# Kernel tuning notes

Hardware: AMD Instinct MI355X
Metric: run time of the kernel (lower is better)

The kernel has to match this reference:

```python
import jax, jax.numpy as jnp
import numpy as np

# NF4 16-level codebook (bitsandbytes values)
NF4_CODEBOOK = jnp.array([
    -1.0, -0.6961928009986877, -0.5250730514526367, -0.39491748809814453,
    -0.28444138169288635, -0.18477343022823334, -0.09105003625154495, 0.0,
    0.07958029955625534, 0.16093020141124725, 0.24611230194568634,
    0.33791524171829224, 0.44070982933044434, 0.5626170039176941,
    0.7229568362236328, 1.0], dtype=jnp.float32)

GROUP = 64      # quant_group_size for NF4
R = 16          # LoRA rank
ALPHA = 16      # lora_alpha -> scaling = ALPHA / R = 1.0
E, H, I, T, TOPK = 8, 2048, 1024, 512, 2


def nf4_dequant_gkn(packed, scales, K, N):
    """packed: [E, K//2, N] uint8-valued ints (two 4-bit codes per byte along K).
    scales: [E, K//GROUP, N] float32 per-group absmax. Returns [E, K, N] fp32."""
    e = packed.shape[0]
    lo = packed & 15
    hi = (packed >> 4) & 15
    codes = jnp.stack([lo, hi], axis=2).reshape(e, K, N)      # interleave along K
    w = NF4_CODEBOOK[codes]                                    # [E, K, N]
    w = w.reshape(e, K // GROUP, GROUP, N) * scales[:, :, None, :]
    return w.reshape(e, K, N)


def setup_inputs() -> dict:
    key = jax.random.key(0)
    ks = jax.random.split(key, 16)
    lora_std = 1.0 / np.sqrt(H)
    return {
        "x": jax.random.normal(ks[0], (T, H), jnp.float32),
        "topk_idx": jax.random.randint(ks[1], (T, TOPK), 0, E, jnp.int32),
        "topk_w": jax.random.uniform(ks[2], (T, TOPK), jnp.float32),
        "gate_packed": jax.random.randint(ks[3], (E, H // 2, I), 0, 256, jnp.int32),
        "gate_scales": jax.random.uniform(ks[4], (E, H // GROUP, I), jnp.float32) * 0.02,
        "up_packed": jax.random.randint(ks[5], (E, H // 2, I), 0, 256, jnp.int32),
        "up_scales": jax.random.uniform(ks[6], (E, H // GROUP, I), jnp.float32) * 0.02,
        "down_packed": jax.random.randint(ks[7], (E, I // 2, H), 0, 256, jnp.int32),
        "down_scales": jax.random.uniform(ks[8], (E, I // GROUP, H), jnp.float32) * 0.02,
        "gate_A": jax.random.normal(ks[9], (E, H, R), jnp.float32) * lora_std,
        "gate_B": jax.random.normal(ks[10], (E, R, I), jnp.float32) * 0.02,
        "up_A": jax.random.normal(ks[11], (E, H, R), jnp.float32) * lora_std,
        "up_B": jax.random.normal(ks[12], (E, R, I), jnp.float32) * 0.02,
        "down_A": jax.random.normal(ks[13], (E, I, R), jnp.float32) * lora_std,
        "down_B": jax.random.normal(ks[14], (E, R, H), jnp.float32) * 0.02,
    }


def reference(x, topk_idx, topk_w, gate_packed, gate_scales, up_packed, up_scales,
              down_packed, down_scales, gate_A, gate_B, up_A, up_B, down_A, down_B):
    scaling = ALPHA / R
    # Dequantized NF4 base + LoRA delta, GKN layout [E, K, N]
    Wg = nf4_dequant_gkn(gate_packed, gate_scales, H, I) + scaling * jnp.einsum('ekr,ern->ekn', gate_A, gate_B)
    Wu = nf4_dequant_gkn(up_packed, up_scales, H, I) + scaling * jnp.einsum('ekr,ern->ekn', up_A, up_B)
    Wd = nf4_dequant_gkn(down_packed, down_scales, I, H) + scaling * jnp.einsum('ekr,ern->ekn', down_A, down_B)
    # Grouped GEMM (dense-over-experts reference): SwiGLU per expert
    g = jnp.einsum('th,ehi->eti', x, Wg)          # [E, T, I]
    u = jnp.einsum('th,ehi->eti', x, Wu)
    h = jax.nn.silu(g) * u
    o = jnp.einsum('eti,eih->eth', h, Wd)         # [E, T, H]
    # Routing combine: per-token per-expert weight from top-k assignments
    w_te = jnp.sum((topk_idx[:, :, None] == jnp.arange(E)) * topk_w[:, :, None], axis=1)  # [T, E]
    return jnp.einsum('eth,te->th', o, w_te)
```

## Files before the change

### kernel.cpp

```cpp
#include <hip/hip_runtime.h>
#include <math.h>

#define NE 8
#define NH 2048
#define NI 1024
#define NT 512
#define NTOPK 2
#define NR 16
#define NGROUP 64
#define NPAIR (NT*NTOPK)

#define SPG 1040
#define SPD 528

typedef short bf16x8 __attribute__((ext_vector_type(8)));
typedef float f32x16 __attribute__((ext_vector_type(16)));
typedef unsigned int u32;

#define MFMA32 __builtin_amdgcn_mfma_f32_32x32x16_bf16

__device__ const float NF4_TAB[16] = {
    -1.0f, -0.6961928009986877f, -0.5250730514526367f, -0.39491748809814453f,
    -0.28444138169288635f, -0.18477343022823334f, -0.09105003625154495f, 0.0f,
    0.07958029955625534f, 0.16093020141124725f, 0.24611230194568634f,
    0.33791524171829224f, 0.44070982933044434f, 0.5626170039176941f,
    0.7229568362236328f, 1.0f};

#define OFF_EXPOFF 0
#define OFF_TOK    256
#define OFF_EXP    4352
#define OFF_W      8448
#define OFF_XAG    12544
#define OFF_XAU    45312
#define OFF_HA     78080
#define OFF_XCT    131072
#define OFF_GU     4325376
#define OFF_HT     10616832
#define OFF_CG     12713984
#define OFF_CU     21233664
#define OFF_CD     29753344

__device__ inline u32 f2bf(float f) {
    return (__float_as_uint(f) + 0x8000u) >> 16;
}
__device__ inline u32 bfpack2(float a, float b) {
    return ((__float_as_uint(a) + 0x8000u) >> 16) |
           ((__float_as_uint(b) + 0x8000u) & 0xFFFF0000u);
}
__device__ inline bf16x8 asbf(uint4 w) {
    union { uint4 u; bf16x8 b; } c; c.u = w; return c.b;
}
__device__ inline bf16x8 bfzero() { return asbf(make_uint4(0,0,0,0)); }
__device__ inline float bf2f(u32 v) { return __uint_as_float(v << 16); }

__device__ __forceinline__ void stage16(const void* g, void* l) {
    __builtin_amdgcn_global_load_lds(
        (const __attribute__((address_space(1))) u32*)g,
        (__attribute__((address_space(3))) u32*)l, 16, 0, 0);
}
#define WAITV0()  asm volatile("s_waitcnt vmcnt(0)" ::: "memory")

__global__ __launch_bounds__(256) void k_cmp3(const u32* __restrict__ gin,
                                              const u32* __restrict__ uin,
                                              const u32* __restrict__ din,
                                              unsigned char* __restrict__ cg,
                                              unsigned char* __restrict__ cu,
                                              unsigned char* __restrict__ cd,
                                              const int* __restrict__ idx,
                                              const float* __restrict__ w,
                                              int* expert_off, int* ptok,
                                              int* pexp, float* pw) {
    __shared__ u32 tile32[32][33];
    __shared__ int cnt[NE], off2[NE + 1], cur[NE];
    int tid = threadIdx.x;
    int z = blockIdx.z;

    if (z == 24) {
        if (blockIdx.x || blockIdx.y) return;
        if (tid < NE) cnt[tid] = 0;
        __syncthreads();
        int e4[4]; float w4[4];
        #pragma unroll
        for (int i = 0; i < 4; ++i) {
            int pr = tid * 4 + i;
            e4[i] = idx[pr]; w4[i] = w[pr];
            atomicAdd(&cnt[e4[i]], 1);
        }
        __syncthreads();
        if (tid == 0) {
            off2[0] = 0;
            for (int i = 0; i < NE; i++) off2[i + 1] = off2[i] + cnt[i];
        }
        __syncthreads();
        if (tid < NE) cur[tid] = off2[tid];
        __syncthreads();
        #pragma unroll
        for (int i = 0; i < 4; ++i) {
            int pr = tid * 4 + i;
            int pos = atomicAdd(&cur[e4[i]], 1);
            ptok[pos] = pr >> 1; pexp[pos] = e4[i]; pw[pos] = w4[i];
        }
        if (tid <= NE) expert_off[tid] = off2[tid];
        return;
    }

    const u32* in; unsigned char* out; int K2, N, SP, e;
    if (z < 2 * NE) {
        e = z >> 1;
        in = (z & 1) ? uin : gin; out = (z & 1) ? cu : cg;
        K2 = NH / 2; N = NI; SP = SPG;
        if ((int)blockIdx.x >= N / 128) return;
    } else {
        e = z - 2 * NE;
        in = din; out = cd;
        K2 = NI / 2; N = NH; SP = SPD;
        if ((int)blockIdx.y >= K2 / 32) return;
    }
    int kp0 = blockIdx.y * 32, c0 = blockIdx.x * 128;

    int c16 = tid & 31, rr = tid >> 5;
    const u32* ip = in + (size_t)e * K2 * N + (size_t)kp0 * N + c0;
    #pragma unroll
    for (int pass = 0; pass < 4; ++pass) {
        int r = pass * 8 + rr;
        uint4 v = *(const uint4*)(ip + (size_t)r * N + c16 * 4);
        tile32[r][c16] = (v.x & 255) | ((v.y & 255) << 8) |
                         ((v.z & 255) << 16) | ((v.w & 255) << 24);
    }
    __syncthreads();

    int col = tid >> 1, half = tid & 1;
    int cq = col >> 2, sh = (col & 3) * 8;
    uint4 ow; u32* op = &ow.x;
    #pragma unroll
    for (int i = 0; i < 4; ++i) {
        int base = half * 16 + i * 4;
        u32 b0 = (tile32[base + 0][cq] >> sh) & 255;
        u32 b1 = (tile32[base + 1][cq] >> sh) & 255;
        u32 b2 = (tile32[base + 2][cq] >> sh) & 255;
        u32 b3 = (tile32[base + 3][cq] >> sh) & 255;
        op[i] = b0 | (b1 << 8) | (b2 << 16) | (b3 << 24);
    }
    *(uint4*)(out + (size_t)e * N * SP + (size_t)(c0 + col) * SP
              + kp0 + half * 16) = ow;
}

__global__ __launch_bounds__(256) void k_xA(const float* __restrict__ x,
                                            const float* __restrict__ gA,
                                            const float* __restrict__ uA,
                                            const int* __restrict__ ptok,
                                            const int* __restrict__ pexp,
                                            unsigned short* __restrict__ xcT,
                                            unsigned short* __restrict__ xAg,
                                            unsigned short* __restrict__ xAu) {
    __shared__ float xs[NH];
    __shared__ float red[2][64][17];
    int p = blockIdx.x;
    int t = ptok[p], e = pexp[p];
    int tid = threadIdx.x;

    int k = tid * 8;
    const float* xr = x + (size_t)t * NH + k;
    float4 v0 = *(const float4*)xr;
    float4 v1 = *(const float4*)(xr + 4);
    uint4 w;
    w.x = bfpack2(v0.x, v0.y); w.y = bfpack2(v0.z, v0.w);
    w.z = bfpack2(v1.x, v1.y); w.w = bfpack2(v1.z, v1.w);
    *(uint4*)(xcT + ((size_t)(k >> 3) * NPAIR + p) * 8) = w;
    *(float4*)(xs + k) = v0;
    *(float4*)(xs + k + 4) = v1;
    __syncthreads();

    int ch = tid & 63, rg = tid >> 6;
    const float* gAr = gA + (size_t)e * NH * NR + rg * 4;
    const float* uAr = uA + (size_t)e * NH * NR + rg * 4;
    float4 sg = make_float4(0.f, 0.f, 0.f, 0.f);
    float4 su = make_float4(0.f, 0.f, 0.f, 0.f);
    #pragma unroll 4
    for (int jj = 0; jj < NH / 64; ++jj) {
        int j = jj * 64 + ch;
        float xv = xs[j];
        float4 ga = *(const float4*)(gAr + (size_t)j * NR);
        float4 ua = *(const float4*)(uAr + (size_t)j * NR);
        sg.x += xv * ga.x; sg.y += xv * ga.y; sg.z += xv * ga.z; sg.w += xv * ga.w;
        su.x += xv * ua.x; su.y += xv * ua.y; su.z += xv * ua.z; su.w += xv * ua.w;
    }
    red[0][ch][rg * 4 + 0] = sg.x; red[0][ch][rg * 4 + 1] = sg.y;
    red[0][ch][rg * 4 + 2] = sg.z; red[0][ch][rg * 4 + 3] = sg.w;
    red[1][ch][rg * 4 + 0] = su.x; red[1][ch][rg * 4 + 1] = su.y;
    red[1][ch][rg * 4 + 2] = su.z; red[1][ch][rg * 4 + 3] = su.w;
    __syncthreads();
    for (int st = 32; st >= 1; st >>= 1) {
        if (ch < st) {
            #pragma unroll
            for (int i = 0; i < 4; ++i) {
                red[0][ch][rg * 4 + i] += red[0][ch + st][rg * 4 + i];
                red[1][ch][rg * 4 + i] += red[1][ch + st][rg * 4 + i];
            }
        }
        __syncthreads();
    }
    if (tid < 16)
        xAg[p * NR + tid] = (unsigned short)f2bf(red[0][0][tid]);
    else if (tid < 32)
        xAu[p * NR + (tid - 16)] = (unsigned short)f2bf(red[1][0][tid - 16]);
}

__global__ __launch_bounds__(64, 3) void k_gu(
    const unsigned short* __restrict__ xcT,
    const unsigned char* __restrict__ cgp, const float* __restrict__ gsc,
    const unsigned char* __restrict__ cup, const float* __restrict__ usc,
    const float* __restrict__ gB, const float* __restrict__ uB,
    const unsigned short* __restrict__ xAg, const unsigned short* __restrict__ xAu,
    const int* __restrict__ expert_off,
    unsigned short* __restrict__ gu)
{
    __shared__ u32 lut[256];
    __shared__ float sclb[32][32];

    int lane = threadIdx.x;
    int q = lane >> 5, cw = lane & 31;
    for (int i = lane; i < 256; i += 64)
        lut[i] = bfpack2(NF4_TAB[i & 15], NF4_TAB[(i >> 4) & 15]);

    int e = blockIdx.x;
    int c0 = blockIdx.y * 32;
    int mat = blockIdx.z & 1;
    int rt = blockIdx.z >> 1;
    const unsigned char* cp = mat ? cup : cgp;
    const float* scp = mat ? usc : gsc;
    const float* Bp = mat ? uB : gB;
    const unsigned short* xA = mat ? xAu : xAg;

    int off = expert_off[e];
    int cnt = expert_off[e + 1] - off;
    int colg = c0 + cw;

    {
        const float* sg = scp + (size_t)e * (NH / NGROUP) * NI + c0;
        #pragma unroll
        for (int g = 0; g < 4; ++g)
            stage16(sg + (size_t)(g * 8 + (lane >> 3)) * NI + ((lane & 7) << 2),
                    &sclb[g * 8][0]);
    }
    WAITV0();

    const unsigned char* cb = cp + ((size_t)e * NI + colg) * SPG + (q << 4);

    const int NS = NH / 64;
    for (int s0 = rt * 32; s0 < cnt; s0 += 128) {
        int rr = s0 + cw; if (rr > cnt - 1) rr = cnt - 1;
        int prow = off + rr;

        auto loadC = [&](uint4& c, int s) {
            c = *(const uint4*)(cb + (s << 5));
        };
        auto loadA = [&](bf16x8* d, int s) {
            #pragma unroll
            for (int ks = 0; ks < 4; ++ks)
                d[ks] = *(const bf16x8*)(xcT +
                            ((size_t)((s << 3) + (q << 2) + ks) * NPAIR + prow) * 8);
        };

        uint4 C0, C1;
        bf16x8 Aa[4], Ab[4];
        f32x16 acc;
        #pragma unroll
        for (int i = 0; i < 16; ++i) acc[i] = 0.f;

        auto compute = [&](const uint4& cv, const bf16x8* Ar, float scl) {
            const u32* cd = &cv.x;
            f32x16 t;
            #pragma unroll
            for (int i = 0; i < 16; ++i) t[i] = 0.f;
            #pragma unroll
            for (int ks = 0; ks < 4; ++ks) {
                u32 d = cd[ks];
                uint4 w4;
                w4.x = lut[d & 255];
                w4.y = lut[(d >> 8) & 255];
                w4.z = lut[(d >> 16) & 255];
                w4.w = lut[d >> 24];
                t = MFMA32(Ar[ks], asbf(w4), t, 0, 0, 0);
            }
            #pragma unroll
            for (int i = 0; i < 16; ++i) acc[i] += scl * t[i];
        };

        loadC(C0, 0); loadA(Aa, 0);
        loadC(C1, 1); loadA(Ab, 1);
        for (int s = 0; s < NS; s += 2) {
            compute(C0, Aa, sclb[s][cw]);
            if (s + 2 < NS) { loadC(C0, s + 2); loadA(Aa, s + 2); }
            compute(C1, Ab, sclb[s + 1][cw]);
            if (s + 3 < NS) { loadC(C1, s + 3); loadA(Ab, s + 3); }
        }

        {
            bf16x8 la = bfzero();
            if (s0 + cw < cnt)
                la = *(const bf16x8*)(xA + (size_t)(off + s0 + cw) * NR + (q << 3));
            const float* Bq = Bp + ((size_t)e * NR + (q << 3)) * NI + colg;
            uint4 w4; u32* wp = &w4.x;
            #pragma unroll
            for (int i = 0; i < 4; ++i)
                wp[i] = bfpack2(Bq[(2 * i) * NI], Bq[(2 * i + 1) * NI]);
            acc = MFMA32(la, asbf(w4), acc, 0, 0, 0);
        }
        unsigned short* outb = gu + (size_t)mat * NPAIR * NI;
        #pragma unroll
        for (int reg = 0; reg < 16; ++reg) {
            int rloc = (reg & 3) + 8 * (reg >> 2) + (q << 2);
            if (s0 + rloc < cnt)
                outb[(size_t)(off + s0 + rloc) * NI + colg] =
                    (unsigned short)f2bf(acc[reg]);
        }
    }
}

__global__ __launch_bounds__(256) void k_hsw(const unsigned short* __restrict__ gu,
                                             const float* __restrict__ dA,
                                             const int* __restrict__ pexp,
                                             unsigned short* __restrict__ hT,
                                             unsigned short* __restrict__ hA) {
    __shared__ float hs[NI];
    __shared__ float red[64][17];
    int p = blockIdx.x, e = pexp[p];
    int tid = threadIdx.x;

    int i = tid * 4;
    uint2 gv = *(const uint2*)(gu + (size_t)p * NI + i);
    uint2 uv = *(const uint2*)(gu + (size_t)NPAIR * NI + (size_t)p * NI + i);
    const u32* gp = &gv.x; const u32* up = &uv.x;
    uint2 hv; u32* hp = &hv.x;
    float4 h4;
    {
        float g0 = bf2f(gp[0] & 0xFFFFu), g1 = bf2f(gp[0] >> 16);
        float u0 = bf2f(up[0] & 0xFFFFu), u1 = bf2f(up[0] >> 16);
        h4.x = g0 * u0 / (1.f + __expf(-g0));
        h4.y = g1 * u1 / (1.f + __expf(-g1));
        hp[0] = bfpack2(h4.x, h4.y);
        float g2 = bf2f(gp[1] & 0xFFFFu), g3 = bf2f(gp[1] >> 16);
        float u2 = bf2f(up[1] & 0xFFFFu), u3 = bf2f(up[1] >> 16);
        h4.z = g2 * u2 / (1.f + __expf(-g2));
        h4.w = g3 * u3 / (1.f + __expf(-g3));
        hp[1] = bfpack2(h4.z, h4.w);
    }
    *(uint2*)(hT + ((size_t)(i >> 3) * NPAIR + p) * 8 + (i & 7)) = hv;
    *(float4*)(hs + i) = h4;
    __syncthreads();

    int ch = tid & 63, rg = tid >> 6;
    const float* dAr = dA + (size_t)e * NI * NR + rg * 4;
    float4 sv = make_float4(0.f, 0.f, 0.f, 0.f);
    #pragma unroll 4
    for (int jj = 0; jj < NI / 64; ++jj) {
        int j = jj * 64 + ch;
        float hvv = hs[j];
        float4 da = *(const float4*)(dAr + (size_t)j * NR);
        sv.x += hvv * da.x; sv.y += hvv * da.y;
        sv.z += hvv * da.z; sv.w += hvv * da.w;
    }
    red[ch][rg * 4 + 0] = sv.x; red[ch][rg * 4 + 1] = sv.y;
    red[ch][rg * 4 + 2] = sv.z; red[ch][rg * 4 + 3] = sv.w;
    __syncthreads();
    for (int st = 32; st >= 1; st >>= 1) {
        if (ch < st) {
            #pragma unroll
            for (int i2 = 0; i2 < 4; ++i2)
                red[ch][rg * 4 + i2] += red[ch + st][rg * 4 + i2];
        }
        __syncthreads();
    }
    if (tid < 16) hA[p * NR + tid] = (unsigned short)f2bf(red[0][tid]);
}

__global__ __launch_bounds__(64, 3) void k_dn(
    const unsigned short* __restrict__ hT,
    const unsigned char* __restrict__ cdp, const float* __restrict__ dsc,
    const float* __restrict__ dB,
    const unsigned short* __restrict__ hA,
    const int* __restrict__ expert_off, const int* __restrict__ ptok,
    const float* __restrict__ pw,
    float* __restrict__ out)
{
    __shared__ u32 lut[256];
    __shared__ float sclb[16][32];

    int lane = threadIdx.x;
    int q = lane >> 5, cw = lane & 31;
    for (int i = lane; i < 256; i += 64)
        lut[i] = bfpack2(NF4_TAB[i & 15], NF4_TAB[(i >> 4) & 15]);

    int e = blockIdx.x;
    int c0 = blockIdx.y * 32;
    int rt = blockIdx.z;

    int off = expert_off[e];
    int cnt = expert_off[e + 1] - off;
    int colg = c0 + cw;

    {
        const float* sg = dsc + (size_t)e * (NI / NGROUP) * NH + c0;
        #pragma unroll
        for (int g = 0; g < 2; ++g)
            stage16(sg + (size_t)(g * 8 + (lane >> 3)) * NH + ((lane & 7) << 2),
                    &sclb[g * 8][0]);
    }
    WAITV0();

    const unsigned char* cb = cdp + ((size_t)e * NH + colg) * SPD + (q << 4);

    const int NS = NI / 64;
    for (int s0 = rt * 32; s0 < cnt; s0 += 128) {
        int rr = s0 + cw; if (rr > cnt - 1) rr = cnt - 1;
        int prow = off + rr;

        auto loadC = [&](uint4& c, int s) {
            c = *(const uint4*)(cb + (s << 5));
        };
        auto loadA = [&](bf16x8* d, int s) {
            #pragma unroll
            for (int ks = 0; ks < 4; ++ks)
                d[ks] = *(const bf16x8*)(hT +
                            ((size_t)((s << 3) + (q << 2) + ks) * NPAIR + prow) * 8);
        };

        uint4 C0, C1;
        bf16x8 Aa[4], Ab[4];
        f32x16 acc;
        #pragma unroll
        for (int i = 0; i < 16; ++i) acc[i] = 0.f;

        auto compute = [&](const uint4& cv, const bf16x8* Ar, float scl) {
            const u32* cd = &cv.x;
            f32x16 t;
            #pragma unroll
            for (int i = 0; i < 16; ++i) t[i] = 0.f;
            #pragma unroll
            for (int ks = 0; ks < 4; ++ks) {
                u32 d = cd[ks];
                uint4 w4;
                w4.x = lut[d & 255];
                w4.y = lut[(d >> 8) & 255];
                w4.z = lut[(d >> 16) & 255];
                w4.w = lut[d >> 24];
                t = MFMA32(Ar[ks], asbf(w4), t, 0, 0, 0);
            }
            #pragma unroll
            for (int i = 0; i < 16; ++i) acc[i] += scl * t[i];
        };

        loadC(C0, 0); loadA(Aa, 0);
        loadC(C1, 1); loadA(Ab, 1);
        for (int s = 0; s < NS; s += 2) {
            compute(C0, Aa, sclb[s][cw]);
            if (s + 2 < NS) { loadC(C0, s + 2); loadA(Aa, s + 2); }
            compute(C1, Ab, sclb[s + 1][cw]);
            if (s + 3 < NS) { loadC(C1, s + 3); loadA(Ab, s + 3); }
        }

        {
            bf16x8 la = bfzero();
            if (s0 + cw < cnt)
                la = *(const bf16x8*)(hA + (size_t)(off + s0 + cw) * NR + (q << 3));
            const float* Bq = dB + ((size_t)e * NR + (q << 3)) * NH + colg;
            uint4 w4; u32* wp = &w4.x;
            #pragma unroll
            for (int i = 0; i < 4; ++i)
                wp[i] = bfpack2(Bq[(2 * i) * NH], Bq[(2 * i + 1) * NH]);
            acc = MFMA32(la, asbf(w4), acc, 0, 0, 0);
        }
        #pragma unroll
        for (int reg = 0; reg < 16; ++reg) {
            int rloc = (reg & 3) + 8 * (reg >> 2) + (q << 2);
            if (s0 + rloc < cnt) {
                int p = off + s0 + rloc;
                atomicAdd(&out[(size_t)ptok[p] * NH + colg], acc[reg] * pw[p]);
            }
        }
    }
}

extern "C" void kernel_launch(void* const* d_in, const int* in_sizes, int n_in,
                              void* d_out, int out_size, void* d_ws,
                              size_t ws_size, hipStream_t stream) {
    const float* x = (const float*)d_in[0];
    const int* topk_idx = (const int*)d_in[1];
    const float* topk_w = (const float*)d_in[2];
    const int* gate_packed = (const int*)d_in[3];
    const float* gate_scales = (const float*)d_in[4];
    const int* up_packed = (const int*)d_in[5];
    const float* up_scales = (const float*)d_in[6];
    const int* down_packed = (const int*)d_in[7];
    const float* down_scales = (const float*)d_in[8];
    const float* gate_A = (const float*)d_in[9];
    const float* gate_B = (const float*)d_in[10];
    const float* up_A = (const float*)d_in[11];
    const float* up_B = (const float*)d_in[12];
    const float* down_A = (const float*)d_in[13];
    const float* down_B = (const float*)d_in[14];
    float* out = (float*)d_out;

    char* ws = (char*)d_ws;
    int* expert_off = (int*)(ws + OFF_EXPOFF);
    int* ptok = (int*)(ws + OFF_TOK);
    int* pexp = (int*)(ws + OFF_EXP);
    float* pw = (float*)(ws + OFF_W);
    unsigned short* xAg = (unsigned short*)(ws + OFF_XAG);
    unsigned short* xAu = (unsigned short*)(ws + OFF_XAU);
    unsigned short* hA = (unsigned short*)(ws + OFF_HA);
    unsigned short* xcT = (unsigned short*)(ws + OFF_XCT);
    unsigned short* gu = (unsigned short*)(ws + OFF_GU);
    unsigned short* hT = (unsigned short*)(ws + OFF_HT);
    unsigned char* cg = (unsigned char*)(ws + OFF_CG);
    unsigned char* cu = (unsigned char*)(ws + OFF_CU);
    unsigned char* cd = (unsigned char*)(ws + OFF_CD);

    hipMemsetAsync(d_out, 0, (size_t)NT * NH * sizeof(float), stream);

    k_cmp3<<<dim3(16, 32, 25), 256, 0, stream>>>(
        (const u32*)gate_packed, (const u32*)up_packed, (const u32*)down_packed,
        cg, cu, cd, topk_idx, topk_w, expert_off, ptok, pexp, pw);

    k_xA<<<NPAIR, 256, 0, stream>>>(x, gate_A, up_A, ptok, pexp, xcT, xAg, xAu);
    k_gu<<<dim3(NE, NI / 32, 8), 64, 0, stream>>>(
        xcT, cg, gate_scales, cu, up_scales, gate_B, up_B,
        xAg, xAu, expert_off, gu);
    k_hsw<<<NPAIR, 256, 0, stream>>>(gu, down_A, pexp, hT, hA);
    k_dn<<<dim3(NE, NH / 32, 4), 64, 0, stream>>>(
        hT, cd, down_scales, down_B, hA, expert_off, ptok, pw, out);
}
```

Before: 271.1 us.

## Pre-dequantize NF4 weights to scaled bf16 in prepass, simplify GEMM inner loops

New measurement: 632.8 us. +133.4%, slower.

```diff
diff --git a/kernel.cpp b/kernel.cpp
--- a/kernel.cpp
+++ b/kernel.cpp
@@ -9,9 +9,6 @@
 #define NR 16
 #define NGROUP 64
 #define NPAIR (NT*NTOPK)
-
-#define SPG 1040
-#define SPD 528
 
 typedef short bf16x8 __attribute__((ext_vector_type(8)));
 typedef float f32x16 __attribute__((ext_vector_type(16)));
@@ -35,10 +32,10 @@
 #define OFF_HA     78080
 #define OFF_XCT    131072
 #define OFF_GU     4325376
-#define OFF_HT     10616832
-#define OFF_CG     12713984
-#define OFF_CU     21233664
-#define OFF_CD     29753344
+#define OFF_HT     8519680
+#define OFF_WTG    10616832
+#define OFF_WTU    44171264
+#define OFF_WTD    77725696
 
 __device__ inline u32 f2bf(float f) {
     return (__float_as_uint(f) + 0x8000u) >> 16;
@@ -53,24 +50,21 @@
 __device__ inline bf16x8 bfzero() { return asbf(make_uint4(0,0,0,0)); }
 __device__ inline float bf2f(u32 v) { return __uint_as_float(v << 16); }
 
-__device__ __forceinline__ void stage16(const void* g, void* l) {
-    __builtin_amdgcn_global_load_lds(
-        (const __attribute__((address_space(1))) u32*)g,
-        (__attribute__((address_space(3))) u32*)l, 16, 0, 0);
-}
-#define WAITV0()  asm volatile("s_waitcnt vmcnt(0)" ::: "memory")
-
-__global__ __launch_bounds__(256) void k_cmp3(const u32* __restrict__ gin,
-                                              const u32* __restrict__ uin,
-                                              const u32* __restrict__ din,
-                                              unsigned char* __restrict__ cg,
-                                              unsigned char* __restrict__ cu,
-                                              unsigned char* __restrict__ cd,
-                                              const int* __restrict__ idx,
-                                              const float* __restrict__ w,
-                                              int* expert_off, int* ptok,
-                                              int* pexp, float* pw) {
-    __shared__ u32 tile32[32][33];
+__global__ __launch_bounds__(256) void k_deq(const u32* __restrict__ gin,
+                                             const u32* __restrict__ uin,
+                                             const u32* __restrict__ din,
+                                             const float* __restrict__ gsc,
+                                             const float* __restrict__ usc,
+                                             const float* __restrict__ dsc,
+                                             unsigned short* __restrict__ wg,
+                                             unsigned short* __restrict__ wu,
+                                             unsigned short* __restrict__ wd,
+                                             const int* __restrict__ idx,
+                                             const float* __restrict__ w,
+                                             int* expert_off, int* ptok,
+                                             int* pexp, float* pw) {
+    __shared__ float2 lutf[256];
+    __shared__ uint4 tile4[32][32];
     __shared__ int cnt[NE], off2[NE + 1], cur[NE];
     int tid = threadIdx.x;
     int z = blockIdx.z;
@@ -104,45 +98,57 @@
         return;
     }
 
-    const u32* in; unsigned char* out; int K2, N, SP, e;
+    const u32* in; const float* sc; unsigned short* out; int K2, N, e;
     if (z < 2 * NE) {
         e = z >> 1;
-        in = (z & 1) ? uin : gin; out = (z & 1) ? cu : cg;
-        K2 = NH / 2; N = NI; SP = SPG;
+        in = (z & 1) ? uin : gin; sc = (z & 1) ? usc : gsc;
+        out = (z & 1) ? wu : wg;
+        K2 = NH / 2; N = NI;
         if ((int)blockIdx.x >= N / 128) return;
     } else {
         e = z - 2 * NE;
-        in = din; out = cd;
-        K2 = NI / 2; N = NH; SP = SPD;
+        in = din; sc = dsc; out = wd;
+        K2 = NI / 2; N = NH;
         if ((int)blockIdx.y >= K2 / 32) return;
     }
     int kp0 = blockIdx.y * 32, c0 = blockIdx.x * 128;
 
-    int c16 = tid & 31, rr = tid >> 5;
+    lutf[tid] = make_float2(NF4_TAB[tid & 15], NF4_TAB[(tid >> 4) & 15]);
+    __syncthreads();
+
+    int r8 = tid >> 5, c16 = tid & 31;
     const u32* ip = in + (size_t)e * K2 * N + (size_t)kp0 * N + c0;
+    float4 scl = *(const float4*)(sc + (size_t)e * (K2 / 32) * N
+                                  + (size_t)blockIdx.y * N + c0 + c16 * 4);
+    const float* sp = &scl.x;
     #pragma unroll
     for (int pass = 0; pass < 4; ++pass) {
-        int r = pass * 8 + rr;
+        int r = pass * 8 + r8;
         uint4 v = *(const uint4*)(ip + (size_t)r * N + c16 * 4);
-        tile32[r][c16] = (v.x & 255) | ((v.y & 255) << 8) |
-                         ((v.z & 255) << 16) | ((v.w & 255) << 24);
-    }
-    __syncthreads();
-
-    int col = tid >> 1, half = tid & 1;
-    int cq = col >> 2, sh = (col & 3) * 8;
-    uint4 ow; u32* op = &ow.x;
+        const u32* vp = &v.x;
+        uint4 ow; u32* owp = &ow.x;
+        #pragma unroll
+        for (int i = 0; i < 4; ++i) {
+            float2 tv = lutf[vp[i] & 255];
+            owp[i] = bfpack2(tv.x * sp[i], tv.y * sp[i]);
+        }
+        tile4[r][c16] = ow;
+    }
+    __syncthreads();
+
+    int col = tid & 127, ch2 = tid >> 7;
+    const u32* t32 = (const u32*)&tile4[0][0];
     #pragma unroll
-    for (int i = 0; i < 4; ++i) {
-        int base = half * 16 + i * 4;
-        u32 b0 = (tile32[base + 0][cq] >> sh) & 255;
-        u32 b1 = (tile32[base + 1][cq] >> sh) & 255;
-        u32 b2 = (tile32[base + 2][cq] >> sh) & 255;
-        u32 b3 = (tile32[base + 3][cq] >> sh) & 255;
-        op[i] = b0 | (b1 << 8) | (b2 << 16) | (b3 << 24);
-    }
-    *(uint4*)(out + (size_t)e * N * SP + (size_t)(c0 + col) * SP
-              + kp0 + half * 16) = ow;
+    for (int j = 0; j < 4; ++j) {
+        int cc = ch2 * 4 + j;
+        uint4 ow;
+        ow.x = t32[(cc * 4 + 0) * 128 + col];
+        ow.y = t32[(cc * 4 + 1) * 128 + col];
+        ow.z = t32[(cc * 4 + 2) * 128 + col];
+        ow.w = t32[(cc * 4 + 3) * 128 + col];
+        *(uint4*)(out + (((size_t)e * (K2 / 4) + (kp0 >> 2) + cc) * N
+                         + (c0 + col)) * 8) = ow;
+    }
 }
 
 __global__ __launch_bounds__(256) void k_xA(const float* __restrict__ x,
@@ -208,27 +214,20 @@
 
 __global__ __launch_bounds__(64, 3) void k_gu(
     const unsigned short* __restrict__ xcT,
-    const unsigned char* __restrict__ cgp, const float* __restrict__ gsc,
-    const unsigned char* __restrict__ cup, const float* __restrict__ usc,
+    const unsigned short* __restrict__ wg,
+    const unsigned short* __restrict__ wu,
     const float* __restrict__ gB, const float* __restrict__ uB,
     const unsigned short* __restrict__ xAg, const unsigned short* __restrict__ xAu,
     const int* __restrict__ expert_off,
     unsigned short* __restrict__ gu)
 {
-    __shared__ u32 lut[256];
-    __shared__ float sclb[32][32];
-
     int lane = threadIdx.x;
     int q = lane >> 5, cw = lane & 31;
-    for (int i = lane; i < 256; i += 64)
-        lut[i] = bfpack2(NF4_TAB[i & 15], NF4_TAB[(i >> 4) & 15]);
 
     int e = blockIdx.x;
     int c0 = blockIdx.y * 32;
     int mat = blockIdx.z & 1;
     int rt = blockIdx.z >> 1;
-    const unsigned char* cp = mat ? cup : cgp;
-    const float* scp = mat ? usc : gsc;
     const float* Bp = mat ? uB : gB;
     const unsigned short* xA = mat ? xAu : xAg;
 
@@ -236,24 +235,20 @@
     int cnt = expert_off[e + 1] - off;
     int colg = c0 + cw;
 
-    {
-        const float* sg = scp + (size_t)e * (NH / NGROUP) * NI + c0;
-        #pragma unroll
-        for (int g = 0; g < 4; ++g)
-            stage16(sg + (size_t)(g * 8 + (lane >> 3)) * NI + ((lane & 7) << 2),
-                    &sclb[g * 8][0]);
-    }
-    WAITV0();
-
-    const unsigned char* cb = cp + ((size_t)e * NI + colg) * SPG + (q << 4);
+    const unsigned short* wbase = (mat ? wu : wg)
+        + (size_t)e * (NH / 8) * (size_t)NI * 8
+        + ((size_t)(q << 2) * NI + colg) * 8;
 
     const int NS = NH / 64;
     for (int s0 = rt * 32; s0 < cnt; s0 += 128) {
         int rr = s0 + cw; if (rr > cnt - 1) rr = cnt - 1;
         int prow = off + rr;
 
-        auto loadC = [&](uint4& c, int s) {
-            c = *(const uint4*)(cb + (s << 5));
+        auto loadW = [&](bf16x8* d, int s) {
+            #pragma unroll
+            for (int ks = 0; ks < 4; ++ks)
+                d[ks] = *(const bf16x8*)(wbase +
+                            (size_t)((s << 3) + ks) * NI * 8);
         };
         auto loadA = [&](bf16x8* d, int s) {
             #pragma unroll
@@ -262,38 +257,24 @@
                             ((size_t)((s << 3) + (q << 2) + ks) * NPAIR + prow) * 8);
         };
 
-        uint4 C0, C1;
-        bf16x8 Aa[4], Ab[4];
+        bf16x8 Aa[4], Ab[4], Wa[4], Wb[4];
         f32x16 acc;
         #pragma unroll
         for (int i = 0; i < 16; ++i) acc[i] = 0.f;
 
-        auto compute = [&](const uint4& cv, const bf16x8* Ar, float scl) {
-            const u32* cd = &cv.x;
-            f32x16 t;
-            #pragma unroll
-            for (int i = 0; i < 16; ++i) t[i] = 0.f;
-            #pragma unroll
-            for (int ks = 0; ks < 4; ++ks) {
-                u32 d = cd[ks];
-                uint4 w4;
-                w4.x = lut[d & 255];
-                w4.y = lut[(d >> 8) & 255];
-                w4.z = lut[(d >> 16) & 255];
-                w4.w = lut[d >> 24];
-                t = MFMA32(Ar[ks], asbf(w4), t, 0, 0, 0);
-            }
-            #pragma unroll
-            for (int i = 0; i < 16; ++i) acc[i] += scl * t[i];
-        };
-
-        loadC(C0, 0); loadA(Aa, 0);
-        loadC(C1, 1); loadA(Ab, 1);
+        auto compute = [&](const bf16x8* Ar, const bf16x8* Wr) {
+            #pragma unroll
+            for (int ks = 0; ks < 4; ++ks)
+                acc = MFMA32(Ar[ks], Wr[ks], acc, 0, 0, 0);
+        };
+
+        loadW(Wa, 0); loadA(Aa, 0);
+        loadW(Wb, 1); loadA(Ab, 1);
         for (int s = 0; s < NS; s += 2) {
-            compute(C0, Aa, sclb[s][cw]);
-            if (s + 2 < NS) { loadC(C0, s + 2); loadA(Aa, s + 2); }
-            compute(C1, Ab, sclb[s + 1][cw]);
-            if (s + 3 < NS) { loadC(C1, s + 3); loadA(Ab, s + 3); }
+            compute(Aa, Wa);
+            if (s + 2 < NS) { loadW(Wa, s + 2); loadA(Aa, s + 2); }
+            compute(Ab, Wb);
+            if (s + 3 < NS) { loadW(Wb, s + 3); loadA(Ab, s + 3); }
         }
 
         {
@@ -377,20 +358,15 @@
 
 __global__ __launch_bounds__(64, 3) void k_dn(
     const unsigned short* __restrict__ hT,
-    const unsigned char* __restrict__ cdp, const float* __restrict__ dsc,
+    const unsigned short* __restrict__ wd,
     const float* __restrict__ dB,
     const unsigned short* __restrict__ hA,
     const int* __restrict__ expert_off, const int* __restrict__ ptok,
     const float* __restrict__ pw,
     float* __restrict__ out)
 {
-    __shared__ u32 lut[256];
-    __shared__ float sclb[16][32];
-
     int lane = threadIdx.x;
     int q = lane >> 5, cw = lane & 31;
-    for (int i = lane; i < 256; i += 64)
-        lut[i] = bfpack2(NF4_TAB[i & 15], NF4_TAB[(i >> 4) & 15]);
 
     int e = blockIdx.x;
     int c0 = blockIdx.y * 32;
@@ -400,24 +376,20 @@
     int cnt = expert_off[e + 1] - off;
     int colg = c0 + cw;
 
-    {
-        const float* sg = dsc + (size_t)e * (NI / NGROUP) * NH + c0;
-        #pragma unroll
-        for (int g = 0; g < 2; ++g)
-            stage16(sg + (size_t)(g * 8 + (lane >> 3)) * NH + ((lane & 7) << 2),
-                    &sclb[g * 8][0]);
-    }
-    WAITV0();
-
-    const unsigned char* cb = cdp + ((size_t)e * NH + colg) * SPD + (q << 4);
+    const unsigned short* wbase = wd
+        + (size_t)e * (NI / 8) * (size_t)NH * 8
+        + ((size_t)(q << 2) * NH + colg) * 8;
 
     const int NS = NI / 64;
     for (int s0 = rt * 32; s0 < cnt; s0 += 128) {
         int rr = s0 + cw; if (rr > cnt - 1) rr = cnt - 1;
         int prow = off + rr;
 
-        auto loadC = [&](uint4& c, int s) {
-            c = *(const uint4*)(cb + (s << 5));
+        auto loadW = [&](bf16x8* d, int s) {
+            #pragma unroll
+            for (int ks = 0; ks < 4; ++ks)
+                d[ks] = *(const bf16x8*)(wbase +
+                            (size_t)((s << 3) + ks) * NH * 8);
         };
         auto loadA = [&](bf16x8* d, int s) {
             #pragma unroll
@@ -426,38 +398,24 @@
                             ((size_t)((s << 3) + (q << 2) + ks) * NPAIR + prow) * 8);
         };
 
-        uint4 C0, C1;
-        bf16x8 Aa[4], Ab[4];
+        bf16x8 Aa[4], Ab[4], Wa[4], Wb[4];
         f32x16 acc;
         #pragma unroll
         for (int i = 0; i < 16; ++i) acc[i] = 0.f;
 
-        auto compute = [&](const uint4& cv, const bf16x8* Ar, float scl) {
-            const u32* cd = &cv.x;
-            f32x16 t;
-            #pragma unroll
-            for (int i = 0; i < 16; ++i) t[i] = 0.f;
-            #pragma unroll
-            for (int ks = 0; ks < 4; ++ks) {
-                u32 d = cd[ks];
-                uint4 w4;
-                w4.x = lut[d & 255];
-                w4.y = lut[(d >> 8) & 255];
-                w4.z = lut[(d >> 16) & 255];
-                w4.w = lut[d >> 24];
-                t = MFMA32(Ar[ks], asbf(w4), t, 0, 0, 0);
-            }
-            #pragma unroll
-            for (int i = 0; i < 16; ++i) acc[i] += scl * t[i];
-        };
-
-        loadC(C0, 0); loadA(Aa, 0);
-        loadC(C1, 1); loadA(Ab, 1);
+        auto compute = [&](const bf16x8* Ar, const bf16x8* Wr) {
+            #pragma unroll
+            for (int ks = 0; ks < 4; ++ks)
+                acc = MFMA32(Ar[ks], Wr[ks], acc, 0, 0, 0);
+        };
+
+        loadW(Wa, 0); loadA(Aa, 0);
+        loadW(Wb, 1); loadA(Ab, 1);
         for (int s = 0; s < NS; s += 2) {
-            compute(C0, Aa, sclb[s][cw]);
-            if (s + 2 < NS) { loadC(C0, s + 2); loadA(Aa, s + 2); }
-            compute(C1, Ab, sclb[s + 1][cw]);
-            if (s + 3 < NS) { loadC(C1, s + 3); loadA(Ab, s + 3); }
+            compute(Aa, Wa);
+            if (s + 2 < NS) { loadW(Wa, s + 2); loadA(Aa, s + 2); }
+            compute(Ab, Wb);
+            if (s + 3 < NS) { loadW(Wb, s + 3); loadA(Ab, s + 3); }
         }
 
         {
@@ -513,21 +471,21 @@
     unsigned short* xcT = (unsigned short*)(ws + OFF_XCT);
     unsigned short* gu = (unsigned short*)(ws + OFF_GU);
     unsigned short* hT = (unsigned short*)(ws + OFF_HT);
-    unsigned char* cg = (unsigned char*)(ws + OFF_CG);
-    unsigned char* cu = (unsigned char*)(ws + OFF_CU);
-    unsigned char* cd = (unsigned char*)(ws + OFF_CD);
+    unsigned short* wtg = (unsigned short*)(ws + OFF_WTG);
+    unsigned short* wtu = (unsigned short*)(ws + OFF_WTU);
+    unsigned short* wtd = (unsigned short*)(ws + OFF_WTD);
 
     hipMemsetAsync(d_out, 0, (size_t)NT * NH * sizeof(float), stream);
 
-    k_cmp3<<<dim3(16, 32, 25), 256, 0, stream>>>(
+    k_deq<<<dim3(16, 32, 25), 256, 0, stream>>>(
         (const u32*)gate_packed, (const u32*)up_packed, (const u32*)down_packed,
-        cg, cu, cd, topk_idx, topk_w, expert_off, ptok, pexp, pw);
+        gate_scales, up_scales, down_scales, wtg, wtu, wtd,
+        topk_idx, topk_w, expert_off, ptok, pexp, pw);
 
     k_xA<<<NPAIR, 256, 0, stream>>>(x, gate_A, up_A, ptok, pexp, xcT, xAg, xAu);
     k_gu<<<dim3(NE, NI / 32, 8), 64, 0, stream>>>(
-        xcT, cg, gate_scales, cu, up_scales, gate_B, up_B,
-        xAg, xAu, expert_off, gu);
+        xcT, wtg, wtu, gate_B, up_B, xAg, xAu, expert_off, gu);
     k_hsw<<<NPAIR, 256, 0, stream>>>(gu, down_A, pexp, hT, hA);
     k_dn<<<dim3(NE, NH / 32, 4), 64, 0, stream>>>(
-        hT, cd, down_scales, down_B, hA, expert_off, ptok, pw, out);
-}
+        hT, wtd, down_B, hA, expert_off, ptok, pw, out);
+}
```
